# Kernel optimization log

Hardware: AMD Instinct MI355X
Metric: run time of the kernel (lower is better)

Reference implementation:

```python
import jax, jax.numpy as jnp
import numpy as np
from jax import lax

B, L, DM = 1, 2048, 1024   # batch, seq len, d_model
N = 16                     # d_state
K = 4                      # d_conv
DI = 2 * DM                # d_inner = d_model * expand_factor


def silu(v):
    return v * jax.nn.sigmoid(v)


def setup_inputs() -> dict:
    key = jax.random.key(0)
    ks = jax.random.split(key, 11)
    s = 0.02
    f32 = jnp.float32
    return {
        "x": jax.random.normal(ks[0], (B, L, DM), f32),
        "W_in": jax.random.normal(ks[1], (2 * DI, DM), f32) * s,
        "b_in": jnp.zeros((2 * DI,), f32),
        "W_conv": jax.random.normal(ks[2], (DI, 1, K), f32) * s,  # depthwise conv kernel (torch layout)
        "b_conv": jnp.zeros((DI,), f32),
        "W_x": jax.random.normal(ks[3], (DI + 2 * N, DI), f32) * s,
        "b_x": jnp.zeros((DI + 2 * N,), f32),
        "W_out": jax.random.normal(ks[4], (DM, DI), f32) * s,
        "b_out": jnp.zeros((DM,), f32),
        "A_log": jax.random.normal(ks[5], (DI, N), f32),
        "D": jnp.ones((DI,), f32),
    }


def reference(x, W_in, b_in, W_conv, b_conv, W_x, b_x, W_out, b_out, A_log, D):
    Bsz = x.shape[0]
    # in_proj and split into ssm branch / residual gate branch
    xr = x @ W_in.T + b_in                      # (B, L, 2*DI)
    xi, res = jnp.split(xr, 2, axis=-1)
    # causal depthwise conv1d: torch pads (K-1) both sides then slices [:L] == left-pad K-1
    xc = jnp.transpose(xi, (0, 2, 1))           # (B, DI, L)
    xc = lax.conv_general_dilated(
        xc, W_conv, window_strides=(1,), padding=[(K - 1, 0)],
        dimension_numbers=("NCH", "OIH", "NCH"), feature_group_count=DI,
    ) + b_conv[None, :, None]
    xi = silu(jnp.transpose(xc, (0, 2, 1)))     # (B, L, DI)
    # selective-scan parameterization
    proj = xi @ W_x.T + b_x                      # (B, L, DI + 2N)
    delta = jax.nn.softplus(proj[..., :DI])      # (B, L, DI)
    B_ssm = proj[..., DI:DI + N]                 # (B, L, N)
    C_ssm = proj[..., DI + N:]                   # (B, L, N)
    A = -jnp.exp(A_log)                          # (DI, N)
    dA = jnp.exp(delta[..., None] * A)                               # (B, L, DI, N)
    dBx = delta[..., None] * B_ssm[:, :, None, :] * xi[..., None]    # (B, L, DI, N)

    def step(h, inp):
        da, dbx, c = inp
        h = da * h + dbx                         # (B, DI, N)
        y = jnp.einsum("bdn,bn->bd", h, c)
        return h, y

    h0 = jnp.zeros((Bsz, DI, N), x.dtype)
    _, ys = lax.scan(
        step, h0,
        (jnp.swapaxes(dA, 0, 1), jnp.swapaxes(dBx, 0, 1), jnp.swapaxes(C_ssm, 0, 1)),
    )
    y = jnp.swapaxes(ys, 0, 1) + xi * D          # skip connection
    y = y * silu(res)                            # gate
    return y @ W_out.T + b_out                   # (B, L, DM)
```

## Files before the change

kernel.cpp:

```cpp
#include <hip/hip_runtime.h>
#include <stdint.h>

#define L_SEQ 2048
#define DMODEL 1024
#define DI_DIM 2048
#define NSSM 16
#define NPROJ 2080
#define NCHUNK 64
#define LCHUNK 32

typedef __attribute__((ext_vector_type(8))) short bf16x8;
typedef __attribute__((ext_vector_type(4))) float f32x4;

__device__ __forceinline__ float bf2f(unsigned short u) {
  union { uint32_t u; float f; } v; v.u = (uint32_t)u << 16; return v.f;
}
__device__ __forceinline__ unsigned short f2bf(float f) {
  union { float f; uint32_t u; } v; v.f = f;
  uint32_t u = v.u;
  return (unsigned short)((u + 0x7fffu + ((u >> 16) & 1u)) >> 16);
}
__device__ __forceinline__ void async16(const void* g, void* l) {
  __builtin_amdgcn_global_load_lds(
      (__attribute__((address_space(1))) void*)(g),
      (__attribute__((address_space(3))) void*)(l), 16, 0, 0);
}
__device__ __forceinline__ float softplusf(float p) {
  return (p > 20.f) ? p : __logf(1.f + __expf(p));
}
__device__ __forceinline__ float siluf(float x) {
  return x * __builtin_amdgcn_rcpf(1.f + __expf(-x));
}

#define WAITV(N) asm volatile("s_waitcnt vmcnt(" #N ")" ::: "memory")
#define GBAR()                                   \
  {                                              \
    __builtin_amdgcn_s_barrier();                \
    asm volatile("" ::: "memory");               \
  }

#define CVT_N1 524288
#define CVT_N2 (CVT_N1 + 1048576)
#define CVT_N3 (CVT_N2 + 1064960)
__global__ void k_convert3(const float* __restrict__ x, const float* __restrict__ win,
                           const float* __restrict__ wx, unsigned short* __restrict__ xb,
                           unsigned short* __restrict__ winb, unsigned short* __restrict__ wxb) {
  int i = blockIdx.x * 256 + threadIdx.x;
  const float4* src; unsigned short* dst; int j;
  if (i < CVT_N1)      { src = (const float4*)x;   dst = xb;   j = i; }
  else if (i < CVT_N2) { src = (const float4*)win; dst = winb; j = i - CVT_N1; }
  else if (i < CVT_N3) { src = (const float4*)wx;  dst = wxb;  j = i - CVT_N2; }
  else return;
  float4 v = src[j];
  ushort4 o;
  o.x = f2bf(v.x); o.y = f2bf(v.y); o.z = f2bf(v.z); o.w = f2bf(v.w);
  ((ushort4*)dst)[j] = o;
}

__global__ void k_f32_to_bf16(const float* __restrict__ in,
                              unsigned short* __restrict__ out, int n4) {
  int i = blockIdx.x * blockDim.x + threadIdx.x;
  if (i < n4) {
    const float4 v = ((const float4*)in)[i];
    ushort4 o;
    o.x = f2bf(v.x); o.y = f2bf(v.y); o.z = f2bf(v.z); o.w = f2bf(v.w);
    ((ushort4*)out)[i] = o;
  }
}

template <typename OutT, int DEPTH>
__global__ __launch_bounds__(256) void k_gemm_bt(
    const unsigned short* __restrict__ A, const unsigned short* __restrict__ B,
    const float* __restrict__ bias, OutT* __restrict__ C,
    int M, int N, int K) {
  __shared__ unsigned short As[DEPTH][64 * 32];
  __shared__ unsigned short Bs[DEPTH][128 * 32];
  const int tid = threadIdx.x;
  const int wave = tid >> 6;
  const int lane = tid & 63;
  const int m0 = blockIdx.y * 64;
  const int n0 = blockIdx.x * 128;
  const int kLen = K / gridDim.z;
  const int kLo = blockIdx.z * kLen;

  const int srow = lane >> 2;
  const int scol = ((lane & 3) ^ ((lane >> 3) & 3)) * 8;
  int ar = m0 + wave * 16 + srow;         if (ar > M - 1) ar = M - 1;
  int br0 = n0 + wave * 32 + srow;        if (br0 > N - 1) br0 = N - 1;
  int br1 = n0 + wave * 32 + 16 + srow;   if (br1 > N - 1) br1 = N - 1;
  const unsigned short* ap  = A + (size_t)ar * K + scol + kLo;
  const unsigned short* bp0 = B + (size_t)br0 * K + scol + kLo;
  const unsigned short* bp1 = B + (size_t)br1 * K + scol + kLo;
  const int soA  = wave * 512;
  const int soB0 = (wave * 2) * 512;
  const int soB1 = (wave * 2 + 1) * 512;

  const int mrow = lane & 15;
  const int swz8 = (((lane >> 4) ^ ((mrow >> 1) & 3)) * 8);
  const int ro = mrow * 32 + swz8;

  f32x4 acc[4][2];
#pragma unroll
  for (int i = 0; i < 4; i++)
#pragma unroll
    for (int j = 0; j < 2; j++) acc[i][j] = (f32x4){0.f, 0.f, 0.f, 0.f};

  const int niter = kLen / 32;

#define STAGE(BUF, KT)                                                         \
  {                                                                            \
    async16(ap + (KT), &As[BUF][soA]);                                         \
    async16(bp0 + (KT), &Bs[BUF][soB0]);                                       \
    async16(bp1 + (KT), &Bs[BUF][soB1]);                                       \
  }

#define GEMM_COMPUTE(BUF)                                                      \
  {                                                                            \
    bf16x8 af[4], bfv[2];                                                      \
    _Pragma("unroll")                                                          \
    for (int i = 0; i < 4; i++)                                                \
      af[i] = *(const bf16x8*)&As[BUF][i * 512 + ro];                          \
    _Pragma("unroll")                                                          \
    for (int j = 0; j < 2; j++)                                                \
      bfv[j] = *(const bf16x8*)&Bs[BUF][(wave * 2 + j) * 512 + ro];            \
    _Pragma("unroll")                                                          \
    for (int i = 0; i < 4; i++)                                                \
      _Pragma("unroll")                                                        \
      for (int j = 0; j < 2; j++)                                              \
        acc[i][j] = __builtin_amdgcn_mfma_f32_16x16x32_bf16(af[i], bfv[j],     \
                                                        acc[i][j], 0, 0, 0);   \
  }

#pragma unroll
  for (int j = 0; j < DEPTH - 1; j++) STAGE(j, j * 32)

  int cur = 0, nxt = DEPTH - 1;
  for (int t = 0; t < niter - (DEPTH - 1); t++) {
    if constexpr (DEPTH == 4) { WAITV(6); } else { WAITV(3); }
    GBAR()
    STAGE(nxt, (t + DEPTH - 1) * 32)
    GEMM_COMPUTE(cur)
    cur = (cur == DEPTH - 1) ? 0 : cur + 1;
    nxt = (nxt == DEPTH - 1) ? 0 : nxt + 1;
  }
  if constexpr (DEPTH == 4) {
    WAITV(6); GBAR()
    GEMM_COMPUTE(cur) cur = (cur == 3) ? 0 : cur + 1;
    WAITV(3); GBAR()
    GEMM_COMPUTE(cur) cur = (cur == 3) ? 0 : cur + 1;
    WAITV(0); GBAR()
    GEMM_COMPUTE(cur)
  } else {
    WAITV(3); GBAR()
    GEMM_COMPUTE(cur) cur = (cur == DEPTH - 1) ? 0 : cur + 1;
    WAITV(0); GBAR()
    GEMM_COMPUTE(cur)
  }
#undef STAGE
#undef GEMM_COMPUTE

  const bool withBias = (gridDim.z == 1);
  OutT* Cz = C + (size_t)blockIdx.z * ((size_t)M * N);
#pragma unroll
  for (int j = 0; j < 2; j++) {
    int col = n0 + wave * 32 + j * 16 + (lane & 15);
    if (col < N) {
      float bv = withBias ? bias[col] : 0.f;
#pragma unroll
      for (int i = 0; i < 4; i++) {
        int rbase = m0 + i * 16 + (lane >> 4) * 4;
#pragma unroll
        for (int r = 0; r < 4; r++) {
          float v = acc[i][j][r] + bv;
          if constexpr (sizeof(OutT) == 2)
            Cz[(size_t)(rbase + r) * N + col] = (OutT)f2bf(v);
          else
            Cz[(size_t)(rbase + r) * N + col] = (OutT)v;
        }
      }
    }
  }
}

__global__ void k_reduce_out(const float* __restrict__ part, const float* __restrict__ bias,
                             float* __restrict__ out) {
  int i = blockIdx.x * 256 + threadIdx.x;
  float4 a = ((const float4*)part)[i];
  float4 b = ((const float4*)(part + (size_t)L_SEQ * DMODEL))[i];
  int col = (i * 4) & (DMODEL - 1);
  float4 bb = *(const float4*)&bias[col];
  float4 o;
  o.x = a.x + b.x + bb.x; o.y = a.y + b.y + bb.y;
  o.z = a.z + b.z + bb.z; o.w = a.w + b.w + bb.w;
  ((float4*)out)[i] = o;
}

__global__ void k_conv_silu(const unsigned short* __restrict__ xr,
                            const float* __restrict__ Wc,
                            const float* __restrict__ bc,
                            unsigned short* __restrict__ xcb) {
  int idx = blockIdx.x * blockDim.x + threadIdx.x;
  if (idx >= L_SEQ * DI_DIM) return;
  int t = idx >> 11;
  int d = idx & (DI_DIM - 1);
  float acc = bc[d];
  const float* wd = Wc + d * 4;
  if (t >= 3) acc += bf2f(xr[(size_t)(t - 3) * (2 * DI_DIM) + d]) * wd[0];
  if (t >= 2) acc += bf2f(xr[(size_t)(t - 2) * (2 * DI_DIM) + d]) * wd[1];
  if (t >= 1) acc += bf2f(xr[(size_t)(t - 1) * (2 * DI_DIM) + d]) * wd[2];
  acc += bf2f(xr[(size_t)t * (2 * DI_DIM) + d]) * wd[3];
  xcb[idx] = f2bf(siluf(acc));
}

__global__ __launch_bounds__(256) void k_scan_a(
    const float* __restrict__ proj, const unsigned short* __restrict__ xcb,
    const float* __restrict__ A_log,
    float* __restrict__ Sdelta, float* __restrict__ hstate) {
  __shared__ float Bsh[LCHUNK * NSSM];
  const int d = blockIdx.x * 256 + threadIdx.x;
  const int c = blockIdx.y;
  const int t0 = c * LCHUNK;
  for (int i = threadIdx.x; i < LCHUNK * NSSM; i += 256) {
    int t = i >> 4, n = i & 15;
    Bsh[i] = proj[(size_t)(t0 + t) * NPROJ + DI_DIM + n];
  }
  __syncthreads();
  float Ar[NSSM], h[NSSM];
#pragma unroll
  for (int n = 0; n < NSSM; n++) {
    Ar[n] = -__expf(A_log[d * NSSM + n]);
    h[n] = 0.f;
  }
  const float* pp = proj + (size_t)t0 * NPROJ + d;
  const unsigned short* xp = xcb + (size_t)t0 * DI_DIM + d;
  float p_nxt = pp[0];
  unsigned short x_nxt = xp[0];
  float sd = 0.f;
  for (int t = 0; t < LCHUNK; t++) {
    float p = p_nxt;
    unsigned short xu = x_nxt;
    if (t + 1 < LCHUNK) {
      p_nxt = pp[(size_t)(t + 1) * NPROJ];
      x_nxt = xp[(size_t)(t + 1) * DI_DIM];
    }
    float delta = softplusf(p);
    float dx = delta * bf2f(xu);
    sd += delta;
#pragma unroll
    for (int n = 0; n < NSSM; n++)
      h[n] = __expf(delta * Ar[n]) * h[n] + dx * Bsh[t * NSSM + n];
  }
  Sdelta[(size_t)c * DI_DIM + d] = sd;
#pragma unroll
  for (int n = 0; n < NSSM; n++)
    hstate[((size_t)c * DI_DIM + d) * NSSM + n] = h[n];
}

__global__ void k_scan_b(const float* __restrict__ A_log,
                         const float* __restrict__ Sdelta,
                         float* __restrict__ hstate) {
  int tid = blockIdx.x * 256 + threadIdx.x;
  int d = tid >> 4;
  float A = -__expf(A_log[tid]);
  float carry = 0.f;
  float v_nxt = hstate[tid];
  float s_nxt = Sdelta[d];
  for (int c = 0; c < NCHUNK; c++) {
    float v = v_nxt, s = s_nxt;
    if (c + 1 < NCHUNK) {
      v_nxt = hstate[(size_t)(c + 1) * DI_DIM * NSSM + tid];
      s_nxt = Sdelta[(size_t)(c + 1) * DI_DIM + d];
    }
    hstate[(size_t)c * DI_DIM * NSSM + tid] = carry;
    carry = __expf(A * s) * carry + v;
  }
}

__global__ __launch_bounds__(256) void k_scan_c(
    const float* __restrict__ proj, const unsigned short* __restrict__ xcb,
    const float* __restrict__ A_log, const float* __restrict__ h0,
    const float* __restrict__ Dvec, const unsigned short* __restrict__ xr,
    unsigned short* __restrict__ ybf) {
  __shared__ float Bsh[LCHUNK * NSSM];
  __shared__ float Csh[LCHUNK * NSSM];
  const int d = blockIdx.x * 256 + threadIdx.x;
  const int c = blockIdx.y;
  const int t0 = c * LCHUNK;
  for (int i = threadIdx.x; i < LCHUNK * NSSM; i += 256) {
    int t = i >> 4, n = i & 15;
    Bsh[i] = proj[(size_t)(t0 + t) * NPROJ + DI_DIM + n];
    Csh[i] = proj[(size_t)(t0 + t) * NPROJ + DI_DIM + NSSM + n];
  }
  __syncthreads();
  float Ar[NSSM], h[NSSM];
#pragma unroll
  for (int n = 0; n < NSSM; n++) {
    Ar[n] = -__expf(A_log[d * NSSM + n]);
    h[n] = h0[((size_t)c * DI_DIM + d) * NSSM + n];
  }
  float Dd = Dvec[d];
  const float* pp = proj + (size_t)t0 * NPROJ + d;
  const unsigned short* xp = xcb + (size_t)t0 * DI_DIM + d;
  const unsigned short* rp = xr + (size_t)t0 * (2 * DI_DIM) + DI_DIM + d;
  float p_nxt = pp[0];
  unsigned short x_nxt = xp[0];
  unsigned short r_nxt = rp[0];
  for (int t = 0; t < LCHUNK; t++) {
    float p = p_nxt;
    unsigned short xu = x_nxt, ru = r_nxt;
    if (t + 1 < LCHUNK) {
      p_nxt = pp[(size_t)(t + 1) * NPROJ];
      x_nxt = xp[(size_t)(t + 1) * DI_DIM];
      r_nxt = rp[(size_t)(t + 1) * (2 * DI_DIM)];
    }
    float delta = softplusf(p);
    float xi = bf2f(xu);
    float dx = delta * xi;
    float y = 0.f;
#pragma unroll
    for (int n = 0; n < NSSM; n++) {
      h[n] = __expf(delta * Ar[n]) * h[n] + dx * Bsh[t * NSSM + n];
      y += h[n] * Csh[t * NSSM + n];
    }
    y += xi * Dd;
    y *= siluf(bf2f(ru));
    ybf[(size_t)(t0 + t) * DI_DIM + d] = f2bf(y);
  }
}

extern "C" void kernel_launch(void* const* d_in, const int* in_sizes, int n_in,
                              void* d_out, int out_size, void* d_ws, size_t ws_size,
                              hipStream_t stream) {
  const float* x      = (const float*)d_in[0];
  const float* W_in   = (const float*)d_in[1];
  const float* b_in   = (const float*)d_in[2];
  const float* W_conv = (const float*)d_in[3];
  const float* b_conv = (const float*)d_in[4];
  const float* W_x    = (const float*)d_in[5];
  const float* b_x    = (const float*)d_in[6];
  const float* W_out  = (const float*)d_in[7];
  const float* b_out  = (const float*)d_in[8];
  const float* A_log  = (const float*)d_in[9];
  const float* Dv     = (const float*)d_in[10];
  float* out = (float*)d_out;

  char* ws = (char*)d_ws;
  size_t off = 0;
  auto alloc = [&](size_t bytes) { void* p = ws + off; off += (bytes + 255) & ~(size_t)255; return p; };
  unsigned short* win_bf = (unsigned short*)alloc((size_t)4096 * DMODEL * 2);
  unsigned short* wx_bf  = (unsigned short*)alloc((size_t)NPROJ * DI_DIM * 2);
  unsigned short* x_bf   = (unsigned short*)alloc((size_t)L_SEQ * DMODEL * 2);
  unsigned short* xr_bf  = (unsigned short*)alloc((size_t)L_SEQ * 2 * DI_DIM * 2);
  unsigned short* xcb    = (unsigned short*)alloc((size_t)L_SEQ * DI_DIM * 2);
  float* proj            = (float*)alloc((size_t)L_SEQ * NPROJ * 4);
  float* Sdelta          = (float*)alloc((size_t)NCHUNK * DI_DIM * 4);
  float* hstate          = (float*)alloc((size_t)NCHUNK * DI_DIM * NSSM * 4);
  if (off > ws_size) return;
  unsigned short* ybf     = win_bf;
  unsigned short* wout_bf = x_bf;
  float* part             = proj;

  k_convert3<<<CVT_N3 / 256, 256, 0, stream>>>(x, W_in, W_x, x_bf, win_bf, wx_bf);

  {
    dim3 g(4096 / 128, L_SEQ / 64);
    k_gemm_bt<unsigned short, 3><<<g, 256, 0, stream>>>(x_bf, win_bf, b_in, xr_bf, L_SEQ, 4096, DMODEL);
  }
  k_f32_to_bf16<<<(DMODEL * DI_DIM / 4) / 256, 256, 0, stream>>>(W_out, wout_bf, DMODEL * DI_DIM / 4);
  k_conv_silu<<<(L_SEQ * DI_DIM) / 256, 256, 0, stream>>>(xr_bf, W_conv, b_conv, xcb);
  {
    dim3 g((NPROJ + 127) / 128, L_SEQ / 64);
    k_gemm_bt<float, 4><<<g, 256, 0, stream>>>(xcb, wx_bf, b_x, proj, L_SEQ, NPROJ, DI_DIM);
  }
  {
    dim3 ga(DI_DIM / 256, NCHUNK);
    k_scan_a<<<ga, 256, 0, stream>>>(proj, xcb, A_log, Sdelta, hstate);
    k_scan_b<<<(DI_DIM * NSSM) / 256, 256, 0, stream>>>(A_log, Sdelta, hstate);
    k_scan_c<<<ga, 256, 0, stream>>>(proj, xcb, A_log, hstate, Dv, xr_bf, ybf);
  }
  {
    dim3 g(DMODEL / 128, L_SEQ / 64, 2);
    k_gemm_bt<float, 4><<<g, 256, 0, stream>>>(ybf, wout_bf, b_out, part, L_SEQ, DMODEL, DI_DIM);
    k_reduce_out<<<(L_SEQ * DMODEL / 4) / 256, 256, 0, stream>>>(part, b_out, out);
  }
}
```

Measured before the change: 278.1 us.

## Fuse W_out conversion, vectorize conv/scan I/O, swap GEMM grid order

Folds the W_out bf16 conversion into the single conversion kernel, using a separate workspace buffer when one fits. Swaps the GEMM grid so M tiles run along blockIdx.x, and drops the proj and out GEMMs from 4-deep to 3-deep LDS pipelining. The conv kernel now handles 8 channels per thread with 16-byte loads and stores, scan state is written and read as float4, and k_scan_b batches its chunk loads 8 at a time. The aim is fewer launches and less memory-instruction overhead, at the cost of less load latency hiding in the two deeper GEMMs. The fallback path's convert launch for W_out is odd: its range starts at the x segment, so with that grid it would reconvert x rather than W_out.

```diff
diff --git a/kernel.cpp b/kernel.cpp
--- a/kernel.cpp
+++ b/kernel.cpp
@@ -10,6 +10,7 @@
 #define LCHUNK 32
 
 typedef __attribute__((ext_vector_type(8))) short bf16x8;
+typedef __attribute__((ext_vector_type(8))) unsigned short u16x8;
 typedef __attribute__((ext_vector_type(4))) float f32x4;
 
 __device__ __forceinline__ float bf2f(unsigned short u) {
@@ -42,14 +43,17 @@
 #define CVT_N1 524288
 #define CVT_N2 (CVT_N1 + 1048576)
 #define CVT_N3 (CVT_N2 + 1064960)
-__global__ void k_convert3(const float* __restrict__ x, const float* __restrict__ win,
-                           const float* __restrict__ wx, unsigned short* __restrict__ xb,
-                           unsigned short* __restrict__ winb, unsigned short* __restrict__ wxb) {
+#define CVT_N4 (CVT_N3 + 524288)
+__global__ void k_convert4(const float* __restrict__ x, const float* __restrict__ win,
+                           const float* __restrict__ wx, const float* __restrict__ wout,
+                           unsigned short* __restrict__ xb, unsigned short* __restrict__ winb,
+                           unsigned short* __restrict__ wxb, unsigned short* __restrict__ woutb) {
   int i = blockIdx.x * 256 + threadIdx.x;
   const float4* src; unsigned short* dst; int j;
-  if (i < CVT_N1)      { src = (const float4*)x;   dst = xb;   j = i; }
-  else if (i < CVT_N2) { src = (const float4*)win; dst = winb; j = i - CVT_N1; }
-  else if (i < CVT_N3) { src = (const float4*)wx;  dst = wxb;  j = i - CVT_N2; }
+  if (i < CVT_N1)      { src = (const float4*)x;    dst = xb;    j = i; }
+  else if (i < CVT_N2) { src = (const float4*)win;  dst = winb;  j = i - CVT_N1; }
+  else if (i < CVT_N3) { src = (const float4*)wx;   dst = wxb;   j = i - CVT_N2; }
+  else if (i < CVT_N4) { src = (const float4*)wout; dst = woutb; j = i - CVT_N3; }
   else return;
   float4 v = src[j];
   ushort4 o;
@@ -57,64 +61,14 @@
   ((ushort4*)dst)[j] = o;
 }
 
-__global__ void k_f32_to_bf16(const float* __restrict__ in,
-                              unsigned short* __restrict__ out, int n4) {
-  int i = blockIdx.x * blockDim.x + threadIdx.x;
-  if (i < n4) {
-    const float4 v = ((const float4*)in)[i];
-    ushort4 o;
-    o.x = f2bf(v.x); o.y = f2bf(v.y); o.z = f2bf(v.z); o.w = f2bf(v.w);
-    ((ushort4*)out)[i] = o;
-  }
-}
-
-template <typename OutT, int DEPTH>
-__global__ __launch_bounds__(256) void k_gemm_bt(
-    const unsigned short* __restrict__ A, const unsigned short* __restrict__ B,
-    const float* __restrict__ bias, OutT* __restrict__ C,
-    int M, int N, int K) {
-  __shared__ unsigned short As[DEPTH][64 * 32];
-  __shared__ unsigned short Bs[DEPTH][128 * 32];
-  const int tid = threadIdx.x;
-  const int wave = tid >> 6;
-  const int lane = tid & 63;
-  const int m0 = blockIdx.y * 64;
-  const int n0 = blockIdx.x * 128;
-  const int kLen = K / gridDim.z;
-  const int kLo = blockIdx.z * kLen;
-
-  const int srow = lane >> 2;
-  const int scol = ((lane & 3) ^ ((lane >> 3) & 3)) * 8;
-  int ar = m0 + wave * 16 + srow;         if (ar > M - 1) ar = M - 1;
-  int br0 = n0 + wave * 32 + srow;        if (br0 > N - 1) br0 = N - 1;
-  int br1 = n0 + wave * 32 + 16 + srow;   if (br1 > N - 1) br1 = N - 1;
-  const unsigned short* ap  = A + (size_t)ar * K + scol + kLo;
-  const unsigned short* bp0 = B + (size_t)br0 * K + scol + kLo;
-  const unsigned short* bp1 = B + (size_t)br1 * K + scol + kLo;
-  const int soA  = wave * 512;
-  const int soB0 = (wave * 2) * 512;
-  const int soB1 = (wave * 2 + 1) * 512;
-
-  const int mrow = lane & 15;
-  const int swz8 = (((lane >> 4) ^ ((mrow >> 1) & 3)) * 8);
-  const int ro = mrow * 32 + swz8;
-
-  f32x4 acc[4][2];
-#pragma unroll
-  for (int i = 0; i < 4; i++)
-#pragma unroll
-    for (int j = 0; j < 2; j++) acc[i][j] = (f32x4){0.f, 0.f, 0.f, 0.f};
-
-  const int niter = kLen / 32;
-
-#define STAGE(BUF, KT)                                                         \
+#define GSTAGE(BUF, KT)                                                        \
   {                                                                            \
     async16(ap + (KT), &As[BUF][soA]);                                         \
     async16(bp0 + (KT), &Bs[BUF][soB0]);                                       \
     async16(bp1 + (KT), &Bs[BUF][soB1]);                                       \
   }
 
-#define GEMM_COMPUTE(BUF)                                                      \
+#define GCOMPUTE(BUF)                                                          \
   {                                                                            \
     bf16x8 af[4], bfv[2];                                                      \
     _Pragma("unroll")                                                          \
@@ -131,56 +85,84 @@
                                                         acc[i][j], 0, 0, 0);   \
   }
 
-#pragma unroll
-  for (int j = 0; j < DEPTH - 1; j++) STAGE(j, j * 32)
-
-  int cur = 0, nxt = DEPTH - 1;
-  for (int t = 0; t < niter - (DEPTH - 1); t++) {
-    if constexpr (DEPTH == 4) { WAITV(6); } else { WAITV(3); }
-    GBAR()
-    STAGE(nxt, (t + DEPTH - 1) * 32)
-    GEMM_COMPUTE(cur)
-    cur = (cur == DEPTH - 1) ? 0 : cur + 1;
-    nxt = (nxt == DEPTH - 1) ? 0 : nxt + 1;
-  }
-  if constexpr (DEPTH == 4) {
-    WAITV(6); GBAR()
-    GEMM_COMPUTE(cur) cur = (cur == 3) ? 0 : cur + 1;
-    WAITV(3); GBAR()
-    GEMM_COMPUTE(cur) cur = (cur == 3) ? 0 : cur + 1;
-    WAITV(0); GBAR()
-    GEMM_COMPUTE(cur)
-  } else {
-    WAITV(3); GBAR()
-    GEMM_COMPUTE(cur) cur = (cur == DEPTH - 1) ? 0 : cur + 1;
-    WAITV(0); GBAR()
-    GEMM_COMPUTE(cur)
-  }
-#undef STAGE
-#undef GEMM_COMPUTE
-
-  const bool withBias = (gridDim.z == 1);
-  OutT* Cz = C + (size_t)blockIdx.z * ((size_t)M * N);
-#pragma unroll
-  for (int j = 0; j < 2; j++) {
-    int col = n0 + wave * 32 + j * 16 + (lane & 15);
-    if (col < N) {
-      float bv = withBias ? bias[col] : 0.f;
-#pragma unroll
-      for (int i = 0; i < 4; i++) {
-        int rbase = m0 + i * 16 + (lane >> 4) * 4;
-#pragma unroll
-        for (int r = 0; r < 4; r++) {
-          float v = acc[i][j][r] + bv;
-          if constexpr (sizeof(OutT) == 2)
-            Cz[(size_t)(rbase + r) * N + col] = (OutT)f2bf(v);
-          else
-            Cz[(size_t)(rbase + r) * N + col] = (OutT)v;
-        }
-      }
-    }
-  }
-}
+#define DEFINE_GEMM_BT(NAME, OutT)                                             \
+__global__ __launch_bounds__(256) void NAME(                                   \
+    const unsigned short* __restrict__ A, const unsigned short* __restrict__ B,\
+    const float* __restrict__ bias, OutT* __restrict__ C,                      \
+    int M, int N, int K) {                                                     \
+  __shared__ unsigned short As[3][64 * 32];                                    \
+  __shared__ unsigned short Bs[3][128 * 32];                                   \
+  const int tid = threadIdx.x;                                                 \
+  const int wave = tid >> 6;                                                   \
+  const int lane = tid & 63;                                                   \
+  const int m0 = blockIdx.x * 64;       \
+  const int n0 = blockIdx.y * 128;                                             \
+  const int kLen = K / gridDim.z;                                              \
+  const int kLo = blockIdx.z * kLen;                                           \
+      \
+  const int srow = lane >> 2;                                                  \
+  const int scol = ((lane & 3) ^ ((lane >> 3) & 3)) * 8;                       \
+  int ar = m0 + wave * 16 + srow;         if (ar > M - 1) ar = M - 1;          \
+  int br0 = n0 + wave * 32 + srow;        if (br0 > N - 1) br0 = N - 1;        \
+  int br1 = n0 + wave * 32 + 16 + srow;   if (br1 > N - 1) br1 = N - 1;        \
+  const unsigned short* ap  = A + (size_t)ar * K + scol + kLo;                 \
+  const unsigned short* bp0 = B + (size_t)br0 * K + scol + kLo;                \
+  const unsigned short* bp1 = B + (size_t)br1 * K + scol + kLo;                \
+  const int soA  = wave * 512;                                                 \
+  const int soB0 = (wave * 2) * 512;                                           \
+  const int soB1 = (wave * 2 + 1) * 512;                                       \
+                     \
+  const int mrow = lane & 15;                                                  \
+  const int swz8 = (((lane >> 4) ^ ((mrow >> 1) & 3)) * 8);                    \
+  const int ro = mrow * 32 + swz8;                                             \
+  f32x4 acc[4][2];                                                             \
+  _Pragma("unroll")                                                            \
+  for (int i = 0; i < 4; i++)                                                  \
+    _Pragma("unroll")                                                          \
+    for (int j = 0; j < 2; j++) acc[i][j] = (f32x4){0.f, 0.f, 0.f, 0.f};       \
+  const int niter = kLen / 32;                                                 \
+  _Pragma("unroll")                                                            \
+  for (int j = 0; j < 2; j++) GSTAGE(j, j * 32)                                \
+  int cur = 0, nxt = 2;                                                        \
+  for (int t = 0; t < niter - 2; t++) {                                        \
+    WAITV(3);                                                                  \
+    GBAR()                                                                     \
+    GSTAGE(nxt, (t + 2) * 32)                                                  \
+    GCOMPUTE(cur)                                                              \
+    cur = (cur == 2) ? 0 : cur + 1;                                            \
+    nxt = (nxt == 2) ? 0 : nxt + 1;                                            \
+  }                                                                            \
+  WAITV(3); GBAR()                                                             \
+  GCOMPUTE(cur) cur = (cur == 2) ? 0 : cur + 1;                                \
+  WAITV(0); GBAR()                                                             \
+  GCOMPUTE(cur)                                                                \
+         \
+  const bool withBias = (gridDim.z == 1);                                      \
+  OutT* Cz = C + (size_t)blockIdx.z * ((size_t)M * N);                         \
+  _Pragma("unroll")                                                            \
+  for (int j = 0; j < 2; j++) {                                                \
+    int col = n0 + wave * 32 + j * 16 + (lane & 15);                           \
+    if (col < N) {                                                             \
+      float bv = withBias ? bias[col] : 0.f;                                   \
+      _Pragma("unroll")                                                        \
+      for (int i = 0; i < 4; i++) {                                            \
+        int rbase = m0 + i * 16 + (lane >> 4) * 4;                             \
+        _Pragma("unroll")                                                      \
+        for (int r = 0; r < 4; r++) {                                          \
+          float v = acc[i][j][r] + bv;                                         \
+          if constexpr (sizeof(OutT) == 2)                                     \
+            Cz[(size_t)(rbase + r) * N + col] = (OutT)f2bf(v);                 \
+          else                                                                 \
+            Cz[(size_t)(rbase + r) * N + col] = (OutT)v;                       \
+        }                                                                      \
+      }                                                                        \
+    }                                                                          \
+  }                                                                            \
+}
+
+DEFINE_GEMM_BT(k_gemm_xr, unsigned short)
+DEFINE_GEMM_BT(k_gemm_proj, float)
+DEFINE_GEMM_BT(k_gemm_out, float)
 
 __global__ void k_reduce_out(const float* __restrict__ part, const float* __restrict__ bias,
                              float* __restrict__ out) {
@@ -199,17 +181,27 @@
                             const float* __restrict__ Wc,
                             const float* __restrict__ bc,
                             unsigned short* __restrict__ xcb) {
-  int idx = blockIdx.x * blockDim.x + threadIdx.x;
-  if (idx >= L_SEQ * DI_DIM) return;
-  int t = idx >> 11;
-  int d = idx & (DI_DIM - 1);
-  float acc = bc[d];
-  const float* wd = Wc + d * 4;
-  if (t >= 3) acc += bf2f(xr[(size_t)(t - 3) * (2 * DI_DIM) + d]) * wd[0];
-  if (t >= 2) acc += bf2f(xr[(size_t)(t - 2) * (2 * DI_DIM) + d]) * wd[1];
-  if (t >= 1) acc += bf2f(xr[(size_t)(t - 1) * (2 * DI_DIM) + d]) * wd[2];
-  acc += bf2f(xr[(size_t)t * (2 * DI_DIM) + d]) * wd[3];
-  xcb[idx] = f2bf(siluf(acc));
+  int idx = blockIdx.x * 256 + threadIdx.x;
+  int t = idx >> 8;
+  int d8 = (idx & 255) * 8;
+  const size_t rs = 2 * DI_DIM;
+  u16x8 x0 = (u16x8)(unsigned short)0, x1 = x0, x2 = x0;
+  u16x8 x3 = *(const u16x8*)&xr[(size_t)t * rs + d8];
+  if (t >= 1) x2 = *(const u16x8*)&xr[(size_t)(t - 1) * rs + d8];
+  if (t >= 2) x1 = *(const u16x8*)&xr[(size_t)(t - 2) * rs + d8];
+  if (t >= 3) x0 = *(const u16x8*)&xr[(size_t)(t - 3) * rs + d8];
+  float4 b0 = *(const float4*)&bc[d8];
+  float4 b1 = *(const float4*)&bc[d8 + 4];
+  float bb[8] = {b0.x, b0.y, b0.z, b0.w, b1.x, b1.y, b1.z, b1.w};
+  u16x8 o;
+#pragma unroll
+  for (int j = 0; j < 8; j++) {
+    float4 wd = *(const float4*)&Wc[(size_t)(d8 + j) * 4];
+    float acc = bb[j] + bf2f(x0[j]) * wd.x + bf2f(x1[j]) * wd.y +
+                bf2f(x2[j]) * wd.z + bf2f(x3[j]) * wd.w;
+    o[j] = f2bf(siluf(acc));
+  }
+  *(u16x8*)&xcb[(size_t)t * DI_DIM + d8] = o;
 }
 
 __global__ __launch_bounds__(256) void k_scan_a(
@@ -251,9 +243,11 @@
       h[n] = __expf(delta * Ar[n]) * h[n] + dx * Bsh[t * NSSM + n];
   }
   Sdelta[(size_t)c * DI_DIM + d] = sd;
-#pragma unroll
-  for (int n = 0; n < NSSM; n++)
-    hstate[((size_t)c * DI_DIM + d) * NSSM + n] = h[n];
+  float4* hp = (float4*)&hstate[((size_t)c * DI_DIM + d) * NSSM];
+  hp[0] = (float4){h[0], h[1], h[2], h[3]};
+  hp[1] = (float4){h[4], h[5], h[6], h[7]};
+  hp[2] = (float4){h[8], h[9], h[10], h[11]};
+  hp[3] = (float4){h[12], h[13], h[14], h[15]};
 }
 
 __global__ void k_scan_b(const float* __restrict__ A_log,
@@ -263,16 +257,18 @@
   int d = tid >> 4;
   float A = -__expf(A_log[tid]);
   float carry = 0.f;
-  float v_nxt = hstate[tid];
-  float s_nxt = Sdelta[d];
-  for (int c = 0; c < NCHUNK; c++) {
-    float v = v_nxt, s = s_nxt;
-    if (c + 1 < NCHUNK) {
-      v_nxt = hstate[(size_t)(c + 1) * DI_DIM * NSSM + tid];
-      s_nxt = Sdelta[(size_t)(c + 1) * DI_DIM + d];
+  for (int cb = 0; cb < NCHUNK; cb += 8) {
+    float v[8], s[8];
+#pragma unroll
+    for (int j = 0; j < 8; j++) {
+      v[j] = hstate[(size_t)(cb + j) * DI_DIM * NSSM + tid];
+      s[j] = Sdelta[(size_t)(cb + j) * DI_DIM + d];
     }
-    hstate[(size_t)c * DI_DIM * NSSM + tid] = carry;
-    carry = __expf(A * s) * carry + v;
+#pragma unroll
+    for (int j = 0; j < 8; j++) {
+      hstate[(size_t)(cb + j) * DI_DIM * NSSM + tid] = carry;
+      carry = __expf(A * s[j]) * carry + v[j];
+    }
   }
 }
 
@@ -288,16 +284,21 @@
   const int t0 = c * LCHUNK;
   for (int i = threadIdx.x; i < LCHUNK * NSSM; i += 256) {
     int t = i >> 4, n = i & 15;
-    Bsh[i] = proj[(size_t)(t0 + t) * NPROJ + DI_DIM + n];
-    Csh[i] = proj[(size_t)(t0 + t) * NPROJ + DI_DIM + NSSM + n];
+    size_t ob = (size_t)(t0 + t) * NPROJ + DI_DIM + n;
+    Bsh[i] = proj[ob];
+    Csh[i] = proj[ob + NSSM];
   }
   __syncthreads();
   float Ar[NSSM], h[NSSM];
 #pragma unroll
-  for (int n = 0; n < NSSM; n++) {
+  for (int n = 0; n < NSSM; n++)
     Ar[n] = -__expf(A_log[d * NSSM + n]);
-    h[n] = h0[((size_t)c * DI_DIM + d) * NSSM + n];
-  }
+  const float4* h0p = (const float4*)&h0[((size_t)c * DI_DIM + d) * NSSM];
+  float4 hv0 = h0p[0], hv1 = h0p[1], hv2 = h0p[2], hv3 = h0p[3];
+  h[0] = hv0.x; h[1] = hv0.y; h[2] = hv0.z; h[3] = hv0.w;
+  h[4] = hv1.x; h[5] = hv1.y; h[6] = hv1.z; h[7] = hv1.w;
+  h[8] = hv2.x; h[9] = hv2.y; h[10] = hv2.z; h[11] = hv2.w;
+  h[12] = hv3.x; h[13] = hv3.y; h[14] = hv3.z; h[15] = hv3.w;
   float Dd = Dvec[d];
   const float* pp = proj + (size_t)t0 * NPROJ + d;
   const unsigned short* xp = xcb + (size_t)t0 * DI_DIM + d;
@@ -360,17 +361,34 @@
   unsigned short* wout_bf = x_bf;
   float* part             = proj;
 
-  k_convert3<<<CVT_N3 / 256, 256, 0, stream>>>(x, W_in, W_x, x_bf, win_bf, wx_bf);
-
+  unsigned short* woutb = (unsigned short*)hstate;
+  unsigned short* wout2 = nullptr;
   {
-    dim3 g(4096 / 128, L_SEQ / 64);
-    k_gemm_bt<unsigned short, 3><<<g, 256, 0, stream>>>(x_bf, win_bf, b_in, xr_bf, L_SEQ, 4096, DMODEL);
-  }
-  k_f32_to_bf16<<<(DMODEL * DI_DIM / 4) / 256, 256, 0, stream>>>(W_out, wout_bf, DMODEL * DI_DIM / 4);
-  k_conv_silu<<<(L_SEQ * DI_DIM) / 256, 256, 0, stream>>>(xr_bf, W_conv, b_conv, xcb);
+    size_t need = (size_t)DMODEL * DI_DIM * 2;
+    if (off + need <= ws_size) wout2 = (unsigned short*)alloc(need);
+  }
+  if (wout2) {
+    k_convert4<<<CVT_N4 / 256, 256, 0, stream>>>(x, W_in, W_x, W_out,
+                                                 x_bf, win_bf, wx_bf, wout2);
+    wout_bf = wout2;
+  } else {
+    k_convert4<<<CVT_N3 / 256, 256, 0, stream>>>(x, W_in, W_x, W_out,
+                                                 x_bf, win_bf, wx_bf, wout_bf);
+  }
+
   {
-    dim3 g((NPROJ + 127) / 128, L_SEQ / 64);
-    k_gemm_bt<float, 4><<<g, 256, 0, stream>>>(xcb, wx_bf, b_x, proj, L_SEQ, NPROJ, DI_DIM);
+    dim3 g(L_SEQ / 64, 4096 / 128);
+    k_gemm_xr<<<g, 256, 0, stream>>>(x_bf, win_bf, b_in, xr_bf, L_SEQ, 4096, DMODEL);
+  }
+  if (!wout2) {
+    k_convert4<<<(CVT_N4 - CVT_N3) / 256, 256, 0, stream>>>(
+        W_out - (size_t)CVT_N3 * 4 + (size_t)CVT_N3 * 4, W_in, W_x, W_out,
+        x_bf, win_bf, wx_bf, wout_bf);
+  }
+  k_conv_silu<<<(L_SEQ * DI_DIM / 8) / 256, 256, 0, stream>>>(xr_bf, W_conv, b_conv, xcb);
+  {
+    dim3 g(L_SEQ / 64, (NPROJ + 127) / 128);
+    k_gemm_proj<<<g, 256, 0, stream>>>(xcb, wx_bf, b_x, proj, L_SEQ, NPROJ, DI_DIM);
   }
   {
     dim3 ga(DI_DIM / 256, NCHUNK);
@@ -379,8 +397,8 @@
     k_scan_c<<<ga, 256, 0, stream>>>(proj, xcb, A_log, hstate, Dv, xr_bf, ybf);
   }
   {
-    dim3 g(DMODEL / 128, L_SEQ / 64, 2);
-    k_gemm_bt<float, 4><<<g, 256, 0, stream>>>(ybf, wout_bf, b_out, part, L_SEQ, DMODEL, DI_DIM);
+    dim3 g(L_SEQ / 64, DMODEL / 128, 2);
+    k_gemm_out<<<g, 256, 0, stream>>>(ybf, wout_bf, b_out, part, L_SEQ, DMODEL, DI_DIM);
     k_reduce_out<<<(L_SEQ * DMODEL / 4) / 256, 256, 0, stream>>>(part, b_out, out);
   }
 }
```

Result: faster. 262.1 us (-5.8%).
